# Performance work log

Measured on AMD Instinct MI355X. Metric: run time of the kernel, lower is better.

Reference implementation:

```python
import jax, jax.numpy as jnp
import numpy as np
from jax import lax

NUM_HEADS = 3
HEAD_CH = 64  # in_ch // num_heads = 192 // 3
EPS = 1e-5   # haiku BatchNorm default eps


def _conv_proj(x, dw, scale, offset, pw, stride):
    # DepthwiseConv2D (SAME, no bias) -> BatchNorm (training: batch stats) -> 1x1 Conv (no bias)
    C = x.shape[-1]
    x = lax.conv_general_dilated(
        x, dw, (stride, stride), 'SAME',
        dimension_numbers=('NHWC', 'HWIO', 'NHWC'),
        feature_group_count=C)
    mean = x.mean(axis=(0, 1, 2))
    var = x.var(axis=(0, 1, 2))
    x = (x - mean) * lax.rsqrt(var + EPS) * scale + offset
    return jnp.einsum('bhwc,cd->bhwd', x, pw)  # pointwise 1x1 conv


def _split_heads(x):
    # b H W (h d) -> b h (H W) d
    b, hh, ww, c = x.shape
    return x.reshape(b, hh * ww, NUM_HEADS, HEAD_CH).transpose(0, 2, 1, 3)


def setup_inputs() -> dict:
    key = jax.random.key(0)
    ks = jax.random.split(key, 18)
    B, H, W, C = 16, 56, 56, 192
    Cout = NUM_HEADS * HEAD_CH  # 192
    g = lambda k, shape, s=0.02: jax.random.normal(k, shape, jnp.float32) * s
    return {
        'inputs_q':  jax.random.normal(ks[0], (B, H, W, C), jnp.float32),
        'inputs_kv': jax.random.normal(ks[1], (B, H, W, C), jnp.float32),
        # depthwise kernels (k, k, 1, C)
        'dw_q': g(ks[2], (3, 3, 1, C)), 'dw_k': g(ks[3], (3, 3, 1, C)), 'dw_v': g(ks[4], (3, 3, 1, C)),
        # BN scale/offset per projection
        'scale_q': jnp.ones((C,), jnp.float32), 'offset_q': jnp.zeros((C,), jnp.float32),
        'scale_k': jnp.ones((C,), jnp.float32), 'offset_k': jnp.zeros((C,), jnp.float32),
        'scale_v': jnp.ones((C,), jnp.float32), 'offset_v': jnp.zeros((C,), jnp.float32),
        # pointwise 1x1 conv kernels (C, Cout)
        'pw_q': g(ks[5], (C, Cout)), 'pw_k': g(ks[6], (C, Cout)), 'pw_v': g(ks[7], (C, Cout)),
        # talking-heads mixing matrices (h, h), near-identity init
        'pre_sm':  jnp.eye(NUM_HEADS, dtype=jnp.float32) + g(ks[8], (NUM_HEADS, NUM_HEADS), 0.1),
        'post_sm': jnp.eye(NUM_HEADS, dtype=jnp.float32) + g(ks[9], (NUM_HEADS, NUM_HEADS), 0.1),
        # output linear (no bias)
        'w_out': g(ks[10], (Cout, C)),
    }


def reference(inputs_q, inputs_kv, dw_q, dw_k, dw_v,
              scale_q, offset_q, scale_k, offset_k, scale_v, offset_v,
              pw_q, pw_k, pw_v, pre_sm, post_sm, w_out):
    q = _conv_proj(inputs_q,  dw_q, scale_q, offset_q, pw_q, 1)  # [B,56,56,192]
    k = _conv_proj(inputs_kv, dw_k, scale_k, offset_k, pw_k, 2)  # [B,28,28,192]
    v = _conv_proj(inputs_kv, dw_v, scale_v, offset_v, pw_v, 2)
    B = q.shape[0]
    q = _split_heads(q) / jnp.sqrt(jnp.float32(HEAD_CH))  # [B,h,Lq,d]
    k = _split_heads(k)                                   # [B,h,Lk,d]
    v = _split_heads(v)
    w = jnp.einsum('bhld,bhkd->bhlk', q, k)               # [B,h,Lq,Lk]
    w = jnp.einsum('bhlk,hg->bglk', w, pre_sm)            # pre-softmax talking heads
    w = jax.nn.softmax(w, axis=-1)
    w = jnp.einsum('bhlk,hg->bglk', w, post_sm)           # post-softmax talking heads
    s = jnp.einsum('bhlk,bhkd->bhld', w, v)               # [B,h,Lq,d]
    s = s.transpose(0, 2, 1, 3).reshape(B, -1, NUM_HEADS * HEAD_CH)  # b l (h d)
    return s @ w_out                                      # [B,Lq,192]
```

## Files before the change

kernel.cpp:

```cpp
#include <hip/hip_runtime.h>

using short8 = __attribute__((ext_vector_type(8))) short;
using f32x4  = __attribute__((ext_vector_type(4))) float;

__device__ __forceinline__ short f2bf(float f){
  unsigned u = __float_as_uint(f);
  unsigned r = (u + 0x7FFFu + ((u >> 16) & 1u)) >> 16;
  return (short)r;
}

__device__ __forceinline__ void async_cp16(short* lds, const short* g){
  __builtin_amdgcn_global_load_lds((const __attribute__((address_space(1))) unsigned int*)g,
                                   (__attribute__((address_space(3))) unsigned int*)lds,
                                   16, 0, 0);
}

__global__ __launch_bounds__(384) void k_dw(const float* __restrict__ inq, const float* __restrict__ inkv,
                                            const float* __restrict__ wq, const float* __restrict__ wk,
                                            const float* __restrict__ wv,
                                            short* __restrict__ dqb, short* __restrict__ dkb,
                                            short* __restrict__ dvb, float2* __restrict__ partq,
                                            float2* __restrict__ partk, float2* __restrict__ partv){
  __shared__ float red[4][384];
  int t = threadIdx.x;
  int c = t % 192, strip = t / 192;
  if(blockIdx.x < 896){
    int bid = blockIdx.x; int b = bid / 56, oh = bid % 56;
    float w[9];
#pragma unroll
    for(int i=0;i<9;i++) w[i] = wq[i*192 + c];
    const float* inb = inq + (size_t)b*56*56*192;
    const float* rp[3]; bool rv[3];
#pragma unroll
    for(int kh=0;kh<3;kh++){
      int ih = oh + kh - 1;
      rv[kh] = (ih >= 0 && ih < 56);
      rp[kh] = inb + (size_t)(rv[kh] ? ih : 0)*56*192 + c;
    }
    auto ldc = [&](int kh, int iw)->float{
      return (rv[kh] && iw >= 0 && iw < 56) ? rp[kh][iw*192] : 0.f;
    };
    int ow0 = strip*28;
    float x0[3], x1[3];
#pragma unroll
    for(int kh=0;kh<3;kh++){ x0[kh] = ldc(kh, ow0-1); x1[kh] = ldc(kh, ow0); }
    float lsum = 0.f, lsq = 0.f;
    size_t orow = ((size_t)b*3136 + (size_t)oh*56)*192;
#pragma unroll 1
    for(int j=0;j<28;j++){
      int ow = ow0 + j;
      float x2[3];
#pragma unroll
      for(int kh=0;kh<3;kh++) x2[kh] = ldc(kh, ow+1);
      float acc = 0.f;
#pragma unroll
      for(int kh=0;kh<3;kh++){
        acc = fmaf(x0[kh], w[kh*3+0], acc);
        acc = fmaf(x1[kh], w[kh*3+1], acc);
        acc = fmaf(x2[kh], w[kh*3+2], acc);
      }
      dqb[orow + (size_t)ow*192 + c] = f2bf(acc);
      lsum += acc; lsq = fmaf(acc, acc, lsq);
#pragma unroll
      for(int kh=0;kh<3;kh++){ x0[kh] = x1[kh]; x1[kh] = x2[kh]; }
    }
    red[0][t] = lsum; red[1][t] = lsq;
    __syncthreads();
    if(t < 192){
      float2 o; o.x = lsum + red[0][t+192]; o.y = lsq + red[1][t+192];
      partq[(size_t)bid*192 + t] = o;
    }
  } else {
    int bid = blockIdx.x - 896; int b = bid / 28, oh = bid % 28;
    float wkr[9], wvr[9];
#pragma unroll
    for(int i=0;i<9;i++){ wkr[i] = wk[i*192 + c]; wvr[i] = wv[i*192 + c]; }
    const float* inb = inkv + (size_t)b*56*56*192;
    const float* rp[3]; bool rv[3];
#pragma unroll
    for(int kh=0;kh<3;kh++){
      int ih = 2*oh + kh;
      rv[kh] = (ih < 56);
      rp[kh] = inb + (size_t)(rv[kh] ? ih : 0)*56*192 + c;
    }
    auto ldc = [&](int kh, int iw)->float{
      return (rv[kh] && iw < 56) ? rp[kh][iw*192] : 0.f;
    };
    int ow0 = strip*14;
    float xp[3];
#pragma unroll
    for(int kh=0;kh<3;kh++) xp[kh] = ldc(kh, 2*ow0);
    float ksum=0.f, ksq=0.f, vsum=0.f, vsq=0.f;
    size_t orow = ((size_t)b*784 + (size_t)oh*28)*192;
#pragma unroll 1
    for(int j=0;j<14;j++){
      int ow = ow0 + j;
      float xm[3], xn[3];
#pragma unroll
      for(int kh=0;kh<3;kh++){ xm[kh] = ldc(kh, 2*ow+1); xn[kh] = ldc(kh, 2*ow+2); }
      float ak = 0.f, av = 0.f;
#pragma unroll
      for(int kh=0;kh<3;kh++){
        ak = fmaf(xp[kh], wkr[kh*3+0], ak); ak = fmaf(xm[kh], wkr[kh*3+1], ak); ak = fmaf(xn[kh], wkr[kh*3+2], ak);
        av = fmaf(xp[kh], wvr[kh*3+0], av); av = fmaf(xm[kh], wvr[kh*3+1], av); av = fmaf(xn[kh], wvr[kh*3+2], av);
      }
      dkb[orow + (size_t)ow*192 + c] = f2bf(ak);
      dvb[orow + (size_t)ow*192 + c] = f2bf(av);
      ksum += ak; ksq = fmaf(ak, ak, ksq);
      vsum += av; vsq = fmaf(av, av, vsq);
#pragma unroll
      for(int kh=0;kh<3;kh++) xp[kh] = xn[kh];
    }
    red[0][t]=ksum; red[1][t]=ksq; red[2][t]=vsum; red[3][t]=vsq;
    __syncthreads();
    if(t < 192){
      float2 a; a.x = ksum + red[0][t+192]; a.y = ksq + red[1][t+192];
      partk[(size_t)bid*192 + t] = a;
      float2 o; o.x = vsum + red[2][t+192]; o.y = vsq + red[3][t+192];
      partv[(size_t)bid*192 + t] = o;
    }
  }
}

__global__ __launch_bounds__(192) void k_red(const float2* __restrict__ pq, const float2* __restrict__ pk,
                                             const float2* __restrict__ pv, float2* __restrict__ oq,
                                             float2* __restrict__ ok2, float2* __restrict__ ov2){
  int blk = blockIdx.x, t = threadIdx.x;
  const float2* src; float2* dst;
  if(blk < 8){ src = pq + (size_t)blk*112*192;      dst = oq  + (size_t)blk*192; }
  else if(blk < 12){ src = pk + (size_t)(blk-8)*112*192;  dst = ok2 + (size_t)(blk-8)*192; }
  else { src = pv + (size_t)(blk-12)*112*192; dst = ov2 + (size_t)(blk-12)*192; }
  float s=0.f, q=0.f;
#pragma unroll 8
  for(int i=0;i<112;i++){ float2 v = src[(size_t)i*192 + t]; s += v.x; q += v.y; }
  float2 o; o.x=s; o.y=q; dst[t] = o;
}

__global__ __launch_bounds__(192) void k_fin(const float2* __restrict__ pq, const float2* __restrict__ pk,
                                             const float2* __restrict__ pv,
                                             const float* __restrict__ sq, const float* __restrict__ oq,
                                             const float* __restrict__ sk, const float* __restrict__ ok,
                                             const float* __restrict__ sv, const float* __restrict__ ov,
                                             const float* __restrict__ pwq, const float* __restrict__ pwk,
                                             const float* __restrict__ pwv, const float* __restrict__ wout,
                                             short* __restrict__ Wt, float* __restrict__ bias){
  int p = blockIdx.x, t = threadIdx.x;
  __shared__ float aS[192], bS[192];
  if(p < 3){
    const float2* part = (p==0)?pq:((p==1)?pk:pv);
    int nb = (p==0)?8:4;
    float N = (p==0)?50176.f:12544.f;
    const float* sc = (p==0)?sq:((p==1)?sk:sv);
    const float* of = (p==0)?oq:((p==1)?ok:ov);
    float s=0.f, q2=0.f;
#pragma unroll
    for(int i=0;i<8;i++){ if(i<nb){ float2 v = part[(size_t)i*192 + t]; s += v.x; q2 += v.y; } }
    float mean = s / N;
    float var  = q2 / N - mean*mean;
    float a  = rsqrtf(var + 1e-5f) * sc[t];
    float bv = of[t] - mean*a;
    aS[t] = a; bS[t] = bv;
    __syncthreads();
    const float* pw = (p==0)?pwq:((p==1)?pwk:pwv);
    float qs = (p==0) ? 0.125f : 1.0f;
    float bacc = 0.f;
    for(int cc=0; cc<192; cc++){
      float wv_ = pw[cc*192 + t];
      bacc = fmaf(bS[cc], wv_, bacc);
      Wt[((size_t)p*192 + t)*192 + cc] = f2bf(aS[cc]*wv_*qs);
    }
    bias[p*192 + t] = bacc * qs;
  } else {
    for(int cc=0; cc<192; cc++) Wt[((size_t)3*192 + t)*192 + cc] = f2bf(wout[cc*192 + t]);
    bias[3*192 + t] = 0.f;
  }
}

__global__ __launch_bounds__(256) void k_kv(const short* __restrict__ dkb, const short* __restrict__ dvb,
                                            const short* __restrict__ Wt, const float* __restrict__ bias,
                                            short* __restrict__ kbuf, short* __restrict__ vtb){
  int blk = blockIdx.x;
  bool isV = blk >= 208;
  int pb = isV ? blk - 208 : blk;
  int w = threadIdx.x >> 6, L = threadIdx.x & 63, l16 = L & 15, h4 = L >> 4;
  int row0 = pb*64 + w*16;
  int b = row0 / 832, kk0 = row0 - b*832;
  const short* A = isV ? dvb : dkb;
  const short* Wp = Wt + (isV ? 2 : 1)*36864;
  const float* bp = bias + (isV ? 2 : 1)*192;
  int kkA = kk0 + l16; if(kkA > 783) kkA = 783;
  short8 af[6];
  const short8* arow = (const short8*)(A + (size_t)(b*784 + kkA)*192);
#pragma unroll
  for(int kf=0;kf<6;kf++) af[kf] = arow[kf*4 + h4];
  short* obase = (isV ? vtb : kbuf) + (size_t)b*26*6144;
#pragma unroll
  for(int nt=0;nt<12;nt++){
    f32x4 acc = f32x4{0.f,0.f,0.f,0.f};
    const short8* wrow = (const short8*)(Wp + (size_t)(nt*16 + l16)*192);
#pragma unroll
    for(int kf=0;kf<6;kf++)
      acc = __builtin_amdgcn_mfma_f32_16x16x32_bf16(af[kf], wrow[kf*4 + h4], acc, 0,0,0);
    int col = nt*16 + l16;
    float bv = bp[col];
#pragma unroll
    for(int r=0;r<4;r++){
      int kk = kk0 + h4*4 + r;
      float v = (kk < 784) ? (acc[r] + bv) : 0.f;
      int t = kk >> 5, rr = kk & 31;
      if(!isV) obase[(size_t)t*6144 + (col>>3)*256 + rr*8 + (col&7)] = f2bf(v);
      else     obase[(size_t)t*6144 + (rr>>3)*1536 + col*8 + (rr&7)] = f2bf(v);
    }
  }
}

__global__ __launch_bounds__(256, 2) void k_attn(const short* __restrict__ dq, const short* __restrict__ Wt,
                                                 const float* __restrict__ bias,
                                                 const short* __restrict__ kb, const short* __restrict__ vt,
                                                 const float* __restrict__ pre, const float* __restrict__ post,
                                                 float* __restrict__ outp){
  __shared__ __align__(16) short sS[32256];
  short* sK0 = sS;          short* sK1 = sS + 6144;
  short* sV0 = sS + 12288;  short* sV1 = sS + 18432;
  short* sP  = sS + 24576;
  int bid = blockIdx.x;
  int b  = ((bid & 7) << 1) | ((bid >> 3) & 1);
  int lt = bid >> 4;
  int tid = threadIdx.x; int w = tid >> 6, lane = tid & 63, l16 = lane & 15, h4 = lane >> 4;
  int lw = lt*64 + w*16;
  short* sScr = sS + w*3200;

  {
    short8 af[6];
    const short8* arow = (const short8*)(dq + ((size_t)b*3136 + lw + l16)*192);
#pragma unroll
    for(int kf=0;kf<6;kf++) af[kf] = arow[kf*4 + h4];
#pragma unroll
    for(int nt=0;nt<12;nt++){
      f32x4 acc = f32x4{0.f,0.f,0.f,0.f};
      const short8* wrow = (const short8*)(Wt + (size_t)(nt*16 + l16)*192);
#pragma unroll
      for(int kf=0;kf<6;kf++)
        acc = __builtin_amdgcn_mfma_f32_16x16x32_bf16(af[kf], wrow[kf*4 + h4], acc, 0,0,0);
      float bv = bias[nt*16 + l16];
#pragma unroll
      for(int r=0;r<4;r++) sScr[(h4*4+r)*200 + nt*16 + l16] = f2bf(acc[r] + bv);
    }
  }
  short8 qf[3][2];
#pragma unroll
  for(int h=0;h<3;h++)
#pragma unroll
    for(int kf=0;kf<2;kf++) qf[h][kf] = *(const short8*)&sScr[l16*200 + h*64 + kf*32 + h4*8];

  float pm[3][3];
#pragma unroll
  for(int h=0;h<3;h++)
#pragma unroll
    for(int g=0;g<3;g++) pm[h][g] = pre[h*3+g];

  f32x4 T[3][3][4];
#pragma unroll
  for(int g=0;g<3;g++)
#pragma unroll
    for(int gp=0;gp<3;gp++)
#pragma unroll
      for(int nt=0;nt<4;nt++) T[g][gp][nt] = f32x4{0.f,0.f,0.f,0.f};
  float Zp[3][4];
#pragma unroll
  for(int g=0;g<3;g++)
#pragma unroll
    for(int r=0;r<4;r++) Zp[g][r] = 0.f;

  const short* kgb = kb + (size_t)b*26*6144;
  const short* vgb = vt + (size_t)b*26*6144;
  int soff = (w*192)*8 + 0;

  auto stage = [&](int t, int pb_){
    const short* kg = kgb + (size_t)t*6144 + soff + lane*8;
    const short* vg = vgb + (size_t)t*6144 + soff + lane*8;
    short* kl = (pb_ ? sK1 : sK0) + soff;
    short* vl = (pb_ ? sV1 : sV0) + soff;
#pragma unroll
    for(int j=0;j<3;j++){
      async_cp16(kl + j*512, kg + j*512);
      async_cp16(vl + j*512, vg + j*512);
    }
  };

  __syncthreads();
  stage(0, 0);
  __syncthreads();

  int sPw = w*1920;
#pragma unroll 1
  for(int ks=0; ks<26; ks++){
    if(ks < 25) stage(ks+1, (ks+1)&1);
    const short* sKc = (ks&1) ? sK1 : sK0;
    const short* sVc = (ks&1) ? sV1 : sV0;
#pragma unroll
    for(int nt=0;nt<2;nt++){
      f32x4 a3[3];
#pragma unroll
      for(int h=0;h<3;h++) a3[h] = f32x4{0.f,0.f,0.f,0.f};
#pragma unroll
      for(int h=0;h<3;h++)
#pragma unroll
        for(int kf=0;kf<2;kf++){
          short8 bk = *(const short8*)&sKc[(h*8 + kf*4 + h4)*256 + (nt*16 + l16)*8];
          a3[h] = __builtin_amdgcn_mfma_f32_16x16x32_bf16(qf[h][kf], bk, a3[h], 0,0,0);
        }
      bool valid = (ks*32 + nt*16 + l16) < 784;
#pragma unroll
      for(int r=0;r<4;r++){
        float s0 = a3[0][r], s1 = a3[1][r], s2 = a3[2][r];
#pragma unroll
        for(int g=0;g<3;g++){
          float sm = fmaf(pm[0][g], s0, fmaf(pm[1][g], s1, pm[2][g]*s2));
          float e = valid ? __expf(sm) : 0.f;
          Zp[g][r] += e;
          sP[sPw + g*640 + (h4*4+r)*40 + nt*16 + l16] = f2bf(e);
        }
      }
    }
    short8 pa[3];
#pragma unroll
    for(int g=0;g<3;g++) pa[g] = *(const short8*)&sP[sPw + g*640 + l16*40 + h4*8];
#pragma unroll
    for(int gp=0;gp<3;gp++)
#pragma unroll
      for(int nt=0;nt<4;nt++){
        short8 vb = *(const short8*)&sVc[h4*1536 + (gp*64 + nt*16 + l16)*8];
#pragma unroll
        for(int g=0;g<3;g++)
          T[g][gp][nt] = __builtin_amdgcn_mfma_f32_16x16x32_bf16(pa[g], vb, T[g][gp][nt], 0,0,0);
      }
    __syncthreads();
  }

  float invZ[3][4];
#pragma unroll
  for(int g=0;g<3;g++)
#pragma unroll
    for(int r=0;r<4;r++){
      float z = Zp[g][r];
      z += __shfl_xor(z, 1); z += __shfl_xor(z, 2); z += __shfl_xor(z, 4); z += __shfl_xor(z, 8);
      invZ[g][r] = 1.f / z;
    }
  float po[3][3];
#pragma unroll
  for(int g=0;g<3;g++)
#pragma unroll
    for(int gp=0;gp<3;gp++) po[g][gp] = post[g*3+gp];

#pragma unroll
  for(int gp=0;gp<3;gp++){
    float cg[3][4];
#pragma unroll
    for(int g=0;g<3;g++)
#pragma unroll
      for(int r=0;r<4;r++) cg[g][r] = po[g][gp] * invZ[g][r];
#pragma unroll
    for(int nt=0;nt<4;nt++){
#pragma unroll
      for(int r=0;r<4;r++){
        float u = fmaf(cg[0][r], T[0][gp][nt][r], fmaf(cg[1][r], T[1][gp][nt][r], cg[2][r]*T[2][gp][nt][r]));
        sScr[(h4*4+r)*200 + gp*64 + nt*16 + l16] = f2bf(u);
      }
    }
  }
  short8 uf[6];
#pragma unroll
  for(int kf=0;kf<6;kf++) uf[kf] = *(const short8*)&sScr[l16*200 + kf*32 + h4*8];
  const short* W3 = Wt + 3*36864;
#pragma unroll
  for(int nt=0;nt<12;nt++){
    f32x4 acc = f32x4{0.f,0.f,0.f,0.f};
    const short8* wrow = (const short8*)(W3 + (size_t)(nt*16 + l16)*192);
#pragma unroll
    for(int kf=0;kf<6;kf++)
      acc = __builtin_amdgcn_mfma_f32_16x16x32_bf16(uf[kf], wrow[kf*4 + h4], acc, 0,0,0);
#pragma unroll
    for(int r=0;r<4;r++)
      outp[((size_t)b*3136 + lw + h4*4 + r)*192 + nt*16 + l16] = acc[r];
  }
}

extern "C" void kernel_launch(void* const* d_in, const int* in_sizes, int n_in,
                              void* d_out, int out_size, void* d_ws, size_t ws_size,
                              hipStream_t stream){
  (void)in_sizes; (void)n_in; (void)out_size; (void)ws_size;
  const float* inq  = (const float*)d_in[0];
  const float* inkv = (const float*)d_in[1];
  const float* dwq  = (const float*)d_in[2];
  const float* dwk  = (const float*)d_in[3];
  const float* dwv  = (const float*)d_in[4];
  const float* scq  = (const float*)d_in[5];  const float* ofq = (const float*)d_in[6];
  const float* sck  = (const float*)d_in[7];  const float* ofk = (const float*)d_in[8];
  const float* scv  = (const float*)d_in[9];  const float* ofv = (const float*)d_in[10];
  const float* pwq  = (const float*)d_in[11];
  const float* pwk  = (const float*)d_in[12];
  const float* pwv  = (const float*)d_in[13];
  const float* pre  = (const float*)d_in[14];
  const float* post = (const float*)d_in[15];
  const float* wout = (const float*)d_in[16];

  char* ws = (char*)d_ws;
  size_t off = 0;
  auto alloc = [&](size_t bytes)->void*{ void* p = ws + off; off += (bytes + 255) & ~(size_t)255; return p; };
  short*  dqb  = (short*) alloc(50176ull*192*2);
  short*  dkb  = (short*) alloc(12544ull*192*2);
  short*  dvb  = (short*) alloc(12544ull*192*2);
  short*  kbuf = (short*) alloc(16ull*26*6144*2);
  short*  vtb  = (short*) alloc(16ull*26*6144*2);
  float2* pq   = (float2*)alloc(896ull*192*sizeof(float2));
  float2* pk   = (float2*)alloc(448ull*192*sizeof(float2));
  float2* pv   = (float2*)alloc(448ull*192*sizeof(float2));
  float2* pq2  = (float2*)alloc(8ull*192*sizeof(float2));
  float2* pk2  = (float2*)alloc(4ull*192*sizeof(float2));
  float2* pv2  = (float2*)alloc(4ull*192*sizeof(float2));
  short*  Wt   = (short*) alloc(4ull*192*192*2);
  float*  bias = (float*) alloc(4ull*192*4);

  k_dw<<<1344, 384, 0, stream>>>(inq, inkv, dwq, dwk, dwv, dqb, dkb, dvb, pq, pk, pv);
  k_red<<<16, 192, 0, stream>>>(pq, pk, pv, pq2, pk2, pv2);
  k_fin<<<4, 192, 0, stream>>>(pq2, pk2, pv2, scq, ofq, sck, ofk, scv, ofv, pwq, pwk, pwv, wout, Wt, bias);
  k_kv<<<416, 256, 0, stream>>>(dkb, dvb, Wt, bias, kbuf, vtb);
  k_attn<<<784, 256, 0, stream>>>(dqb, Wt, bias, kbuf, vtb, pre, post, (float*)d_out);
}
```

Measured before the change: 241.9 us.

## Apply post-softmax head mixing before PV using a two-pass softmax

The attention kernel now makes two passes over K. The first pass only accumulates the softmax denominators. The second pass recomputes the scores, normalises them, and applies the post-softmax talking-heads mix before the PV matmul. This shrinks the PV accumulators from 3x3x4 to 3x4 tiles and cuts PV MFMAs by a factor of three, at the cost of computing QK twice. The lower register use and smaller LDS footprint (V is now read directly from global) allow launch bounds of 4 blocks per CU. The loop now covers 25 key tiles instead of 26, and the mixing coefficients are broadcast via readfirstlane.

```diff
diff --git a/kernel.cpp b/kernel.cpp
--- a/kernel.cpp
+++ b/kernel.cpp
@@ -8,7 +8,9 @@
   unsigned r = (u + 0x7FFFu + ((u >> 16) & 1u)) >> 16;
   return (short)r;
 }
-
+__device__ __forceinline__ float sget(float x){
+  return __uint_as_float(__builtin_amdgcn_readfirstlane(__float_as_uint(x)));
+}
 __device__ __forceinline__ void async_cp16(short* lds, const short* g){
   __builtin_amdgcn_global_load_lds((const __attribute__((address_space(1))) unsigned int*)g,
                                    (__attribute__((address_space(3))) unsigned int*)lds,
@@ -214,15 +216,15 @@
   }
 }
 
-__global__ __launch_bounds__(256, 2) void k_attn(const short* __restrict__ dq, const short* __restrict__ Wt,
+__global__ __launch_bounds__(256, 4) void k_attn(const short* __restrict__ dq, const short* __restrict__ Wt,
                                                  const float* __restrict__ bias,
                                                  const short* __restrict__ kb, const short* __restrict__ vt,
                                                  const float* __restrict__ pre, const float* __restrict__ post,
                                                  float* __restrict__ outp){
-  __shared__ __align__(16) short sS[32256];
-  short* sK0 = sS;          short* sK1 = sS + 6144;
-  short* sV0 = sS + 12288;  short* sV1 = sS + 18432;
-  short* sP  = sS + 24576;
+  __shared__ __align__(16) short sS[19968];
+  short* sK0 = sS;
+  short* sK1 = sS + 6144;
+  short* sP  = sS + 12288;
   int bid = blockIdx.x;
   int b  = ((bid & 7) << 1) | ((bid >> 3) & 1);
   int lt = bid >> 4;
@@ -257,47 +259,33 @@
 #pragma unroll
   for(int h=0;h<3;h++)
 #pragma unroll
-    for(int g=0;g<3;g++) pm[h][g] = pre[h*3+g];
-
-  f32x4 T[3][3][4];
-#pragma unroll
-  for(int g=0;g<3;g++)
-#pragma unroll
-    for(int gp=0;gp<3;gp++)
-#pragma unroll
-      for(int nt=0;nt<4;nt++) T[g][gp][nt] = f32x4{0.f,0.f,0.f,0.f};
-  float Zp[3][4];
-#pragma unroll
-  for(int g=0;g<3;g++)
-#pragma unroll
-    for(int r=0;r<4;r++) Zp[g][r] = 0.f;
+    for(int g=0;g<3;g++) pm[h][g] = sget(pre[h*3+g]);
 
   const short* kgb = kb + (size_t)b*26*6144;
   const short* vgb = vt + (size_t)b*26*6144;
-  int soff = (w*192)*8 + 0;
-
-  auto stage = [&](int t, int pb_){
+  int soff = w*1536;
+
+  auto stageK = [&](int t, int pb_){
     const short* kg = kgb + (size_t)t*6144 + soff + lane*8;
-    const short* vg = vgb + (size_t)t*6144 + soff + lane*8;
     short* kl = (pb_ ? sK1 : sK0) + soff;
-    short* vl = (pb_ ? sV1 : sV0) + soff;
-#pragma unroll
-    for(int j=0;j<3;j++){
-      async_cp16(kl + j*512, kg + j*512);
-      async_cp16(vl + j*512, vg + j*512);
-    }
+#pragma unroll
+    for(int j=0;j<3;j++) async_cp16(kl + j*512, kg + j*512);
   };
 
+  float Zp[3][4];
+#pragma unroll
+  for(int g=0;g<3;g++)
+#pragma unroll
+    for(int r=0;r<4;r++) Zp[g][r] = 0.f;
+
   __syncthreads();
-  stage(0, 0);
+  stageK(0, 0);
   __syncthreads();
 
-  int sPw = w*1920;
 #pragma unroll 1
-  for(int ks=0; ks<26; ks++){
-    if(ks < 25) stage(ks+1, (ks+1)&1);
+  for(int ks=0; ks<25; ks++){
+    if(ks < 24) stageK(ks+1, (ks+1)&1);
     const short* sKc = (ks&1) ? sK1 : sK0;
-    const short* sVc = (ks&1) ? sV1 : sV0;
 #pragma unroll
     for(int nt=0;nt<2;nt++){
       f32x4 a3[3];
@@ -317,24 +305,10 @@
 #pragma unroll
         for(int g=0;g<3;g++){
           float sm = fmaf(pm[0][g], s0, fmaf(pm[1][g], s1, pm[2][g]*s2));
-          float e = valid ? __expf(sm) : 0.f;
-          Zp[g][r] += e;
-          sP[sPw + g*640 + (h4*4+r)*40 + nt*16 + l16] = f2bf(e);
+          Zp[g][r] += valid ? __expf(sm) : 0.f;
         }
       }
     }
-    short8 pa[3];
-#pragma unroll
-    for(int g=0;g<3;g++) pa[g] = *(const short8*)&sP[sPw + g*640 + l16*40 + h4*8];
-#pragma unroll
-    for(int gp=0;gp<3;gp++)
-#pragma unroll
-      for(int nt=0;nt<4;nt++){
-        short8 vb = *(const short8*)&sVc[h4*1536 + (gp*64 + nt*16 + l16)*8];
-#pragma unroll
-        for(int g=0;g<3;g++)
-          T[g][gp][nt] = __builtin_amdgcn_mfma_f32_16x16x32_bf16(pa[g], vb, T[g][gp][nt], 0,0,0);
-      }
     __syncthreads();
   }
 
@@ -351,24 +325,71 @@
 #pragma unroll
   for(int g=0;g<3;g++)
 #pragma unroll
-    for(int gp=0;gp<3;gp++) po[g][gp] = post[g*3+gp];
-
-#pragma unroll
-  for(int gp=0;gp<3;gp++){
-    float cg[3][4];
-#pragma unroll
-    for(int g=0;g<3;g++)
-#pragma unroll
-      for(int r=0;r<4;r++) cg[g][r] = po[g][gp] * invZ[g][r];
-#pragma unroll
-    for(int nt=0;nt<4;nt++){
+    for(int gp=0;gp<3;gp++) po[g][gp] = sget(post[g*3+gp]);
+
+  f32x4 U[3][4];
+#pragma unroll
+  for(int gp=0;gp<3;gp++)
+#pragma unroll
+    for(int nt=0;nt<4;nt++) U[gp][nt] = f32x4{0.f,0.f,0.f,0.f};
+
+  stageK(0, 0);
+  __syncthreads();
+
+  int sPw = w*1920;
+#pragma unroll 1
+  for(int ks=0; ks<25; ks++){
+    if(ks < 24) stageK(ks+1, (ks+1)&1);
+    const short* sKc = (ks&1) ? sK1 : sK0;
+#pragma unroll
+    for(int nt=0;nt<2;nt++){
+      f32x4 a3[3];
+#pragma unroll
+      for(int h=0;h<3;h++) a3[h] = f32x4{0.f,0.f,0.f,0.f};
+#pragma unroll
+      for(int h=0;h<3;h++)
+#pragma unroll
+        for(int kf=0;kf<2;kf++){
+          short8 bk = *(const short8*)&sKc[(h*8 + kf*4 + h4)*256 + (nt*16 + l16)*8];
+          a3[h] = __builtin_amdgcn_mfma_f32_16x16x32_bf16(qf[h][kf], bk, a3[h], 0,0,0);
+        }
+      bool valid = (ks*32 + nt*16 + l16) < 784;
 #pragma unroll
       for(int r=0;r<4;r++){
-        float u = fmaf(cg[0][r], T[0][gp][nt][r], fmaf(cg[1][r], T[1][gp][nt][r], cg[2][r]*T[2][gp][nt][r]));
-        sScr[(h4*4+r)*200 + gp*64 + nt*16 + l16] = f2bf(u);
+        float s0 = a3[0][r], s1 = a3[1][r], s2 = a3[2][r];
+        float pn[3];
+#pragma unroll
+        for(int g=0;g<3;g++){
+          float sm = fmaf(pm[0][g], s0, fmaf(pm[1][g], s1, pm[2][g]*s2));
+          pn[g] = (valid ? __expf(sm) : 0.f) * invZ[g][r];
+        }
+#pragma unroll
+        for(int gp=0;gp<3;gp++){
+          float wp = fmaf(po[0][gp], pn[0], fmaf(po[1][gp], pn[1], po[2][gp]*pn[2]));
+          sP[sPw + gp*640 + (h4*4+r)*40 + nt*16 + l16] = f2bf(wp);
+        }
       }
     }
-  }
+    const short* vtile = vgb + (size_t)ks*6144 + h4*1536;
+#pragma unroll
+    for(int gp=0;gp<3;gp++){
+      short8 pa = *(const short8*)&sP[sPw + gp*640 + l16*40 + h4*8];
+#pragma unroll
+      for(int nt=0;nt<4;nt++){
+        short8 vb = *(const short8*)(vtile + (gp*64 + nt*16 + l16)*8);
+        U[gp][nt] = __builtin_amdgcn_mfma_f32_16x16x32_bf16(pa, vb, U[gp][nt], 0,0,0);
+      }
+    }
+    __syncthreads();
+  }
+
+#pragma unroll
+  for(int gp=0;gp<3;gp++)
+#pragma unroll
+    for(int nt=0;nt<4;nt++)
+#pragma unroll
+      for(int r=0;r<4;r++)
+        sScr[(h4*4+r)*200 + gp*64 + nt*16 + l16] = f2bf(U[gp][nt][r]);
   short8 uf[6];
 #pragma unroll
   for(int kf=0;kf<6;kf++) uf[kf] = *(const short8*)&sScr[l16*200 + kf*32 + h4*8];
```

New measurement: 290.3 us. +20.0%, slower.

## Software-pipeline QK and PV across iterations with triple-buffered V tiles

Applied to the files above, without the earlier changes.

Restructures the attention loop so each iteration computes QK scores for the current K tile while running the PV MFMAs for the previous tile, using a triple-buffered V ring and double-buffered K in LDS. The loop runs over 25 tiles instead of 26, with an epilogue PV step, and masking is moved to a zok flag on the row-sum accumulation. It also transposes the QK MFMA operands so each lane holds four keys per row, which allows packed bf16 conversion (v_cvt_pk_bf16_f32) with 8-byte LDS stores and a simpler row-sum reduction. Other changes are exp2f with log2e folded into the pre-mix weights and readfirstlane for the mixing scalars. LDS use grows, which may lower occupancy, and the masking of the padded tail depends on the new tile count and the zok condition.

```diff
diff --git a/kernel.cpp b/kernel.cpp
--- a/kernel.cpp
+++ b/kernel.cpp
@@ -8,7 +8,14 @@
   unsigned r = (u + 0x7FFFu + ((u >> 16) & 1u)) >> 16;
   return (short)r;
 }
-
+__device__ __forceinline__ float sget(float x){
+  return __uint_as_float(__builtin_amdgcn_readfirstlane(__float_as_uint(x)));
+}
+__device__ __forceinline__ unsigned cvtpk_bf16(float lo, float hi){
+  unsigned d;
+  asm("v_cvt_pk_bf16_f32 %0, %1, %2" : "=v"(d) : "v"(lo), "v"(hi));
+  return d;
+}
 __device__ __forceinline__ void async_cp16(short* lds, const short* g){
   __builtin_amdgcn_global_load_lds((const __attribute__((address_space(1))) unsigned int*)g,
                                    (__attribute__((address_space(3))) unsigned int*)lds,
@@ -219,10 +226,10 @@
                                                  const short* __restrict__ kb, const short* __restrict__ vt,
                                                  const float* __restrict__ pre, const float* __restrict__ post,
                                                  float* __restrict__ outp){
-  __shared__ __align__(16) short sS[32256];
-  short* sK0 = sS;          short* sK1 = sS + 6144;
-  short* sV0 = sS + 12288;  short* sV1 = sS + 18432;
-  short* sP  = sS + 24576;
+  __shared__ __align__(16) short sS[38400];
+  short* sKb = sS;
+  short* sVb = sS + 12288;
+  short* sP  = sS + 30720;
   int bid = blockIdx.x;
   int b  = ((bid & 7) << 1) | ((bid >> 3) & 1);
   int lt = bid >> 4;
@@ -257,7 +264,7 @@
 #pragma unroll
   for(int h=0;h<3;h++)
 #pragma unroll
-    for(int g=0;g<3;g++) pm[h][g] = pre[h*3+g];
+    for(int g=0;g<3;g++) pm[h][g] = sget(pre[h*3+g]) * 1.44269504f;
 
   f32x4 T[3][3][4];
 #pragma unroll
@@ -266,21 +273,17 @@
     for(int gp=0;gp<3;gp++)
 #pragma unroll
       for(int nt=0;nt<4;nt++) T[g][gp][nt] = f32x4{0.f,0.f,0.f,0.f};
-  float Zp[3][4];
-#pragma unroll
-  for(int g=0;g<3;g++)
-#pragma unroll
-    for(int r=0;r<4;r++) Zp[g][r] = 0.f;
+  float Zp[3] = {0.f, 0.f, 0.f};
 
   const short* kgb = kb + (size_t)b*26*6144;
   const short* vgb = vt + (size_t)b*26*6144;
-  int soff = (w*192)*8 + 0;
-
-  auto stage = [&](int t, int pb_){
+  int soff = w*1536;
+
+  auto stage = [&](int t){
+    short* kl = sKb + (t&1)*6144 + soff;
+    short* vl = sVb + (t%3)*6144 + soff;
     const short* kg = kgb + (size_t)t*6144 + soff + lane*8;
     const short* vg = vgb + (size_t)t*6144 + soff + lane*8;
-    short* kl = (pb_ ? sK1 : sK0) + soff;
-    short* vl = (pb_ ? sV1 : sV0) + soff;
 #pragma unroll
     for(int j=0;j<3;j++){
       async_cp16(kl + j*512, kg + j*512);
@@ -289,40 +292,65 @@
   };
 
   __syncthreads();
-  stage(0, 0);
+  stage(0);
   __syncthreads();
 
   int sPw = w*1920;
 #pragma unroll 1
-  for(int ks=0; ks<26; ks++){
-    if(ks < 25) stage(ks+1, (ks+1)&1);
-    const short* sKc = (ks&1) ? sK1 : sK0;
-    const short* sVc = (ks&1) ? sV1 : sV0;
+  for(int ks=0; ks<25; ks++){
+    if(ks < 24) stage(ks+1);
+    const short* sKc = sKb + (ks&1)*6144;
+    f32x4 acc[3][2];
+#pragma unroll
+    for(int h=0;h<3;h++)
+#pragma unroll
+      for(int nt=0;nt<2;nt++) acc[h][nt] = f32x4{0.f,0.f,0.f,0.f};
+#pragma unroll
+    for(int h=0;h<3;h++)
+#pragma unroll
+      for(int kf=0;kf<2;kf++){
+        short8 aq = qf[h][kf];
+#pragma unroll
+        for(int nt=0;nt<2;nt++){
+          short8 bk = *(const short8*)&sKc[(h*8 + kf*4 + h4)*256 + (nt*16 + l16)*8];
+          acc[h][nt] = __builtin_amdgcn_mfma_f32_16x16x32_bf16(bk, aq, acc[h][nt], 0,0,0);
+        }
+      }
+    if(ks){
+      const short* sVp = sVb + ((ks-1)%3)*6144 + h4*1536;
+      short8 pa[3];
+#pragma unroll
+      for(int g=0;g<3;g++) pa[g] = *(const short8*)&sP[sPw + g*640 + l16*40 + h4*8];
+#pragma unroll
+      for(int gp=0;gp<3;gp++)
+#pragma unroll
+        for(int nt=0;nt<4;nt++){
+          short8 vb = *(const short8*)(sVp + (gp*64 + nt*16 + l16)*8);
+#pragma unroll
+          for(int g=0;g<3;g++)
+            T[g][gp][nt] = __builtin_amdgcn_mfma_f32_16x16x32_bf16(pa[g], vb, T[g][gp][nt], 0,0,0);
+        }
+    }
 #pragma unroll
     for(int nt=0;nt<2;nt++){
-      f32x4 a3[3];
-#pragma unroll
-      for(int h=0;h<3;h++) a3[h] = f32x4{0.f,0.f,0.f,0.f};
-#pragma unroll
-      for(int h=0;h<3;h++)
-#pragma unroll
-        for(int kf=0;kf<2;kf++){
-          short8 bk = *(const short8*)&sKc[(h*8 + kf*4 + h4)*256 + (nt*16 + l16)*8];
-          a3[h] = __builtin_amdgcn_mfma_f32_16x16x32_bf16(qf[h][kf], bk, a3[h], 0,0,0);
+      bool zok = (ks < 24) || (nt == 0);
+#pragma unroll
+      for(int g=0;g<3;g++){
+        float e[4];
+#pragma unroll
+        for(int r=0;r<4;r++){
+          float sm = fmaf(pm[0][g], acc[0][nt][r], fmaf(pm[1][g], acc[1][nt][r], pm[2][g]*acc[2][nt][r]));
+          e[r] = exp2f(sm);
         }
-      bool valid = (ks*32 + nt*16 + l16) < 784;
-#pragma unroll
-      for(int r=0;r<4;r++){
-        float s0 = a3[0][r], s1 = a3[1][r], s2 = a3[2][r];
-#pragma unroll
-        for(int g=0;g<3;g++){
-          float sm = fmaf(pm[0][g], s0, fmaf(pm[1][g], s1, pm[2][g]*s2));
-          float e = valid ? __expf(sm) : 0.f;
-          Zp[g][r] += e;
-          sP[sPw + g*640 + (h4*4+r)*40 + nt*16 + l16] = f2bf(e);
-        }
-      }
-    }
+        if(zok) Zp[g] += (e[0] + e[1]) + (e[2] + e[3]);
+        uint2 dw; dw.x = cvtpk_bf16(e[0], e[1]); dw.y = cvtpk_bf16(e[2], e[3]);
+        *(uint2*)&sP[sPw + g*640 + l16*40 + nt*16 + h4*4] = dw;
+      }
+    }
+    __syncthreads();
+  }
+  {
+    const short* sVp = sVb + (24%3)*6144 + h4*1536;
     short8 pa[3];
 #pragma unroll
     for(int g=0;g<3;g++) pa[g] = *(const short8*)&sP[sPw + g*640 + l16*40 + h4*8];
@@ -330,28 +358,27 @@
     for(int gp=0;gp<3;gp++)
 #pragma unroll
       for(int nt=0;nt<4;nt++){
-        short8 vb = *(const short8*)&sVc[h4*1536 + (gp*64 + nt*16 + l16)*8];
+        short8 vb = *(const short8*)(sVp + (gp*64 + nt*16 + l16)*8);
 #pragma unroll
         for(int g=0;g<3;g++)
           T[g][gp][nt] = __builtin_amdgcn_mfma_f32_16x16x32_bf16(pa[g], vb, T[g][gp][nt], 0,0,0);
       }
-    __syncthreads();
-  }
-
-  float invZ[3][4];
+  }
+
+  float izq[3][4];
+#pragma unroll
+  for(int g=0;g<3;g++){
+    float z = Zp[g];
+    z += __shfl_xor(z, 16); z += __shfl_xor(z, 32);
+    float iz = 1.f / z;
+#pragma unroll
+    for(int r=0;r<4;r++) izq[g][r] = __shfl(iz, h4*4 + r);
+  }
+  float po[3][3];
 #pragma unroll
   for(int g=0;g<3;g++)
 #pragma unroll
-    for(int r=0;r<4;r++){
-      float z = Zp[g][r];
-      z += __shfl_xor(z, 1); z += __shfl_xor(z, 2); z += __shfl_xor(z, 4); z += __shfl_xor(z, 8);
-      invZ[g][r] = 1.f / z;
-    }
-  float po[3][3];
-#pragma unroll
-  for(int g=0;g<3;g++)
-#pragma unroll
-    for(int gp=0;gp<3;gp++) po[g][gp] = post[g*3+gp];
+    for(int gp=0;gp<3;gp++) po[g][gp] = sget(post[g*3+gp]);
 
 #pragma unroll
   for(int gp=0;gp<3;gp++){
@@ -359,7 +386,7 @@
 #pragma unroll
     for(int g=0;g<3;g++)
 #pragma unroll
-      for(int r=0;r<4;r++) cg[g][r] = po[g][gp] * invZ[g][r];
+      for(int r=0;r<4;r++) cg[g][r] = po[g][gp] * izq[g][r];
 #pragma unroll
     for(int nt=0;nt<4;nt++){
 #pragma unroll
```

Measured after the change: 234.3 us (median of 3 runs). 1.03x faster.
